# Performance work log

Measured on AMD Instinct MI355X. Metric: run time of the kernel, lower is better.

The kernel has to match this reference:

```python
import jax, jax.numpy as jnp
import numpy as np
from jax import lax

N_NODES = 50000
N_EDGES = 800000
FEAT = 16
HID = 64
K = 32
N_CLASSES = 8


def _dconv(Xc, W, b, src, dst, norm_out, norm_in):
    """Dual-direction diffusion (Chebyshev-style) graph convolution.
    Xc: [N, Fin], W: [2, K, Fin, HID], norm_*: per-edge weights."""
    N = Xc.shape[0]

    def prop(x, s, d, ne):
        # out[i] = sum_{e: d[e]=i} ne[e] * x[s[e]]
        return jax.ops.segment_sum(x[s] * ne[:, None], d, num_segments=N)

    # k = 0 term (identity support, both directions)
    H = Xc @ (W[0, 0] + W[1, 0])
    # k = 1 term
    T1o = prop(Xc, src, dst, norm_out)   # forward diffusion
    T1i = prop(Xc, dst, src, norm_in)    # reverse diffusion
    H = H + T1o @ W[0, 1] + T1i @ W[1, 1]

    def step(carry, Wk):
        T0o, T1o, T0i, T1i, Hacc = carry
        T2o = 2.0 * prop(T1o, src, dst, norm_out) - T0o
        T2i = 2.0 * prop(T1i, dst, src, norm_in) - T0i
        Hacc = Hacc + T2o @ Wk[0] + T2i @ Wk[1]
        return (T1o, T2o, T1i, T2i, Hacc), None

    Wtail = jnp.stack([W[0, 2:], W[1, 2:]], axis=1)  # [K-2, 2, Fin, HID]
    (_, _, _, _, H), _ = lax.scan(step, (Xc, T1o, Xc, T1i, H), Wtail)
    return H + b


def setup_inputs() -> dict:
    key = jax.random.key(0)
    ks = jax.random.split(key, 8)
    Fin = FEAT + HID
    wscale = 1.0 / np.sqrt(Fin * K)
    x = jax.random.normal(ks[0], (N_NODES, FEAT), jnp.float32)
    edge_index = jax.random.randint(ks[1], (2, N_EDGES), 0, N_NODES, jnp.int64)
    W_z = jax.random.normal(ks[2], (2, K, Fin, HID), jnp.float32) * wscale
    W_r = jax.random.normal(ks[3], (2, K, Fin, HID), jnp.float32) * wscale
    W_h = jax.random.normal(ks[4], (2, K, Fin, HID), jnp.float32) * wscale
    lin_w = jax.random.normal(ks[5], (HID, N_CLASSES), jnp.float32) / np.sqrt(HID)
    return {
        "x": x, "edge_index": edge_index,
        "W_z": W_z, "b_z": jnp.zeros((HID,), jnp.float32),
        "W_r": W_r, "b_r": jnp.zeros((HID,), jnp.float32),
        "W_h": W_h, "b_h": jnp.zeros((HID,), jnp.float32),
        "lin_w": lin_w, "lin_b": jnp.zeros((N_CLASSES,), jnp.float32),
    }


def reference(x, edge_index, W_z, b_z, W_r, b_r, W_h, b_h, lin_w, lin_b):
    N = x.shape[0]
    src, dst = edge_index[0], edge_index[1]
    w = jnp.ones(src.shape[0], x.dtype)
    deg_out = jax.ops.segment_sum(w, src, num_segments=N)
    deg_in = jax.ops.segment_sum(w, dst, num_segments=N)
    inv = lambda d: jnp.where(d > 0, 1.0 / d, 0.0)
    norm_out = inv(deg_out)[src]  # per-edge 1/out-deg(source), forward walk
    norm_in = inv(deg_in)[dst]    # per-edge 1/in-deg(target), reverse walk

    # DCRNN GRU cell, single step, H initialized to zeros
    H0 = jnp.zeros((N, HID), x.dtype)
    Xc = jnp.concatenate([x, H0], axis=1)
    Z = jax.nn.sigmoid(_dconv(Xc, W_z, b_z, src, dst, norm_out, norm_in))
    R = jax.nn.sigmoid(_dconv(Xc, W_r, b_r, src, dst, norm_out, norm_in))
    Xh = jnp.concatenate([x, H0 * R], axis=1)
    Ht = jnp.tanh(_dconv(Xh, W_h, b_h, src, dst, norm_out, norm_in))
    H = Z * H0 + (1.0 - Z) * Ht

    return jax.nn.relu(H) @ lin_w + lin_b
```

## Files before the change

kernel.cpp:

```cpp
#include <hip/hip_runtime.h>
#include <math.h>

#define N_NODES 50000
#define N_EDGES 800000
#define FEAT    16
#define HID     64
#define KORD    32
#define NCLS    8

#define WSL     5120
#define SLOT    (N_NODES * FEAT)

typedef __attribute__((ext_vector_type(8))) short bf8_t;
typedef __attribute__((ext_vector_type(4))) float f32x4;

static constexpr size_t Aln(size_t x) { return (x + 255) & ~size_t(255); }

static constexpr size_t OFF_DEG_OUT = 0;
static constexpr size_t OFF_DEG_IN  = OFF_DEG_OUT + Aln(N_NODES * 4);
static constexpr size_t OFF_CUR_DST = OFF_DEG_IN  + Aln(N_NODES * 4);
static constexpr size_t OFF_CUR_SRC = OFF_CUR_DST + Aln(N_NODES * 4);
static constexpr size_t ZERO_BYTES  = OFF_CUR_SRC + Aln(N_NODES * 4);
static constexpr size_t OFF_OFF_DST = ZERO_BYTES;
static constexpr size_t OFF_OFF_SRC = OFF_OFF_DST + Aln((N_NODES + 1) * 4);
static constexpr size_t OFF_CSRD    = OFF_OFF_SRC + Aln((N_NODES + 1) * 4);
static constexpr size_t OFF_CSRS    = OFF_CSRD + Aln(N_EDGES * 4);
static constexpr size_t OFF_SLAB    = OFF_CSRS + Aln(N_EDGES * 4);
static constexpr size_t OFF_BSZH    = OFF_SLAB + Aln((size_t)64 * SLOT * 4);
static constexpr size_t OFF_BSZL    = OFF_BSZH + Aln((size_t)32 * 8 * 64 * 8 * 2);
static constexpr size_t WS_TOTAL    = OFF_BSZL + Aln((size_t)32 * 8 * 64 * 8 * 2);

__device__ __forceinline__ ushort f2bf(float v) {
    unsigned int b = __float_as_uint(v);
    b += 0x7FFFu + ((b >> 16) & 1u);
    return (ushort)(b >> 16);
}
__device__ __forceinline__ float bf2f(ushort h) {
    return __uint_as_float((unsigned int)h << 16);
}

__global__ void count_deg_kernel(const int* __restrict__ ei,
                                 int* __restrict__ deg_out, int* __restrict__ deg_in) {
    int e4 = blockIdx.x * blockDim.x + threadIdx.x;
    if (e4 * 4 >= N_EDGES) return;
    int4 s = *(const int4*)&ei[e4 * 4];
    int4 d = *(const int4*)&ei[N_EDGES + e4 * 4];
    atomicAdd(&deg_out[s.x], 1); atomicAdd(&deg_out[s.y], 1);
    atomicAdd(&deg_out[s.z], 1); atomicAdd(&deg_out[s.w], 1);
    atomicAdd(&deg_in[d.x], 1);  atomicAdd(&deg_in[d.y], 1);
    atomicAdd(&deg_in[d.z], 1);  atomicAdd(&deg_in[d.w], 1);
}

__global__ __launch_bounds__(1024) void scan_kernel(const int* __restrict__ degA, int* __restrict__ offA,
                                                    const int* __restrict__ degB, int* __restrict__ offB) {
    const int* deg = blockIdx.x ? degB : degA;
    int* off = blockIdx.x ? offB : offA;
    __shared__ int wsum[16];
    __shared__ int s_run;
    const int t = threadIdx.x, lane = t & 63, wid = t >> 6;
    if (t == 0) s_run = 0;
    __syncthreads();
    for (int base = 0; base < N_NODES; base += 1024) {
        int i = base + t;
        int v = (i < N_NODES) ? deg[i] : 0;
        int xv = v;
        #pragma unroll
        for (int d = 1; d < 64; d <<= 1) {
            int tt = __shfl_up(xv, d, 64);
            if (lane >= d) xv += tt;
        }
        if (lane == 63) wsum[wid] = xv;
        __syncthreads();
        int add = s_run;
        for (int w = 0; w < wid; ++w) add += wsum[w];
        if (i < N_NODES) off[i] = add + xv - v;
        __syncthreads();
        if (t == 1023) s_run = add + xv;
        __syncthreads();
    }
    if (t == 0) off[N_NODES] = s_run;
}

__global__ void fill_csr_kernel(const int* __restrict__ ei,
                                const int* __restrict__ deg_out, const int* __restrict__ deg_in,
                                const int* __restrict__ off_dst, const int* __restrict__ off_src,
                                int* __restrict__ cur_dst, int* __restrict__ cur_src,
                                unsigned int* __restrict__ csrd, unsigned int* __restrict__ csrs) {
    int e = blockIdx.x * blockDim.x + threadIdx.x;
    if (e >= N_EDGES) return;
    int s = ei[e], d = ei[N_EDGES + e];
    int p = off_dst[d] + atomicAdd(&cur_dst[d], 1);
    csrd[p] = ((unsigned int)deg_out[s] << 16) | (unsigned int)s;
    int q = off_src[s] + atomicAdd(&cur_src[s], 1);
    csrs[q] = ((unsigned int)deg_in[d] << 16) | (unsigned int)d;
}

__device__ __forceinline__ float4 gather4d(const unsigned int* __restrict__ csr, int beg, int end,
                                           int u, int fq, const float* __restrict__ src) {
    float4 acc = {0.f, 0.f, 0.f, 0.f};
    for (int e0 = beg; e0 < end; e0 += 16) {
        int ea = e0 + u, eb = e0 + 4 + u, ec = e0 + 8 + u, ed = e0 + 12 + u;
        unsigned int pa = (ea < end) ? csr[ea] : 0x10000u;
        unsigned int pb = (eb < end) ? csr[eb] : 0x10000u;
        unsigned int pc = (ec < end) ? csr[ec] : 0x10000u;
        unsigned int pd = (ed < end) ? csr[ed] : 0x10000u;
        float wa = (ea < end) ? 1.0f / (float)(pa >> 16) : 0.0f;
        float wb = (eb < end) ? 1.0f / (float)(pb >> 16) : 0.0f;
        float wc = (ec < end) ? 1.0f / (float)(pc >> 16) : 0.0f;
        float wd = (ed < end) ? 1.0f / (float)(pd >> 16) : 0.0f;
        const float4 ra = *(const float4*)&src[(pa & 0xFFFFu) * FEAT + fq * 4];
        const float4 rb = *(const float4*)&src[(pb & 0xFFFFu) * FEAT + fq * 4];
        const float4 rc = *(const float4*)&src[(pc & 0xFFFFu) * FEAT + fq * 4];
        const float4 rd = *(const float4*)&src[(pd & 0xFFFFu) * FEAT + fq * 4];
        acc.x += wa * ra.x + wb * rb.x + wc * rc.x + wd * rd.x;
        acc.y += wa * ra.y + wb * rb.y + wc * rc.y + wd * rd.y;
        acc.z += wa * ra.z + wb * rb.z + wc * rc.z + wd * rd.z;
        acc.w += wa * ra.w + wb * rb.w + wc * rc.w + wd * rd.w;
    }
    return acc;
}

__device__ __forceinline__ float4 reduce_u(float4 a) {
    a.x += __shfl_xor(a.x, 4); a.y += __shfl_xor(a.y, 4);
    a.z += __shfl_xor(a.z, 4); a.w += __shfl_xor(a.w, 4);
    a.x += __shfl_xor(a.x, 8); a.y += __shfl_xor(a.y, 8);
    a.z += __shfl_xor(a.z, 8); a.w += __shfl_xor(a.w, 8);
    return a;
}

__global__ __launch_bounds__(256) void init_kernel(
    const float* __restrict__ x,
    const int* __restrict__ off_dst, const unsigned int* __restrict__ csrd,
    const int* __restrict__ off_src, const unsigned int* __restrict__ csrs,
    float* __restrict__ slab) {
    const int dir = blockIdx.x & 1;
    const int bi  = blockIdx.x >> 1;
    const int* off = dir ? off_src : off_dst;
    const unsigned int* csr = dir ? csrs : csrd;
    const int t = threadIdx.x;
    const int g = t >> 4, l = t & 15, u = l >> 2, fq = l & 3;
    const int i = bi * 16 + g;
    const int b = off[i], e = off[i + 1];
    float4 a = reduce_u(gather4d(csr, b, e, u, fq, x));
    if (u == 0) {
        const int ro = i * FEAT + fq * 4;
        float4 xr = *(const float4*)&x[ro];
        *(float4*)&slab[(size_t)(dir * 32 + 0) * SLOT + ro] = xr;
        *(float4*)&slab[(size_t)(dir * 32 + 1) * SLOT + ro] = a;
    }
}

__global__ __launch_bounds__(256) void step_kernel(
    const int* __restrict__ off_dst, const unsigned int* __restrict__ csrd,
    const int* __restrict__ off_src, const unsigned int* __restrict__ csrs,
    float* __restrict__ slab, int k) {
    const int dir = blockIdx.x & 1;
    const int bi  = blockIdx.x >> 1;
    const int* off = dir ? off_src : off_dst;
    const unsigned int* csr = dir ? csrs : csrd;
    const float* prev = slab + (size_t)(dir * 32 + k - 1) * SLOT;
    const float* pp   = slab + (size_t)(dir * 32 + k - 2) * SLOT;
    float*       outp = slab + (size_t)(dir * 32 + k) * SLOT;
    const int t = threadIdx.x;
    const int g = t >> 4, l = t & 15, u = l >> 2, fq = l & 3;
    const int i = bi * 16 + g;
    const int b = off[i], e = off[i + 1];
    float4 a = reduce_u(gather4d(csr, b, e, u, fq, prev));
    if (u == 0) {
        const int ro = i * FEAT + fq * 4;
        float4 p = *(const float4*)&pp[ro];
        float4 t2;
        t2.x = 2.f * a.x - p.x; t2.y = 2.f * a.y - p.y;
        t2.z = 2.f * a.z - p.z; t2.w = 2.f * a.w - p.w;
        *(float4*)&outp[ro] = t2;
    }
}

__global__ void wswiz_kernel(const float* __restrict__ Wz, const float* __restrict__ Wh,
                             ushort* __restrict__ bszh, ushort* __restrict__ bszl) {
    int idx = blockIdx.x * blockDim.x + threadIdx.x;
    if (idx >= 32 * 8 * 64) return;
    int l  = idx & 63;
    int nc = (idx >> 6) & 7;
    int kc = idx >> 9;
    int si = kc * 2 + ((l >> 4) >> 1);
    int f0 = ((l >> 4) & 1) * 8;
    int c  = nc * 16 + (l & 15);
    const float* W = (c < 64) ? Wz : Wh;
    int cc = (c < 64) ? c : c - 64;
    ushort vh[8], vl[8];
    #pragma unroll
    for (int i = 0; i < 8; ++i) {
        float v = W[(size_t)si * WSL + (f0 + i) * 64 + cc];
        ushort h = f2bf(v);
        vh[i] = h;
        vl[i] = f2bf(v - bf2f(h));
    }
    ushort* dh = &bszh[(size_t)idx * 8];
    *(ushort4*)dh       = make_ushort4(vh[0], vh[1], vh[2], vh[3]);
    *(ushort4*)(dh + 4) = make_ushort4(vh[4], vh[5], vh[6], vh[7]);
    ushort* dl = &bszl[(size_t)idx * 8];
    *(ushort4*)dl       = make_ushort4(vl[0], vl[1], vl[2], vl[3]);
    *(ushort4*)(dl + 4) = make_ushort4(vl[4], vl[5], vl[6], vl[7]);
}

__global__ __launch_bounds__(256) void final_kernel(
    const float* __restrict__ slab, const ushort* __restrict__ bszh, const ushort* __restrict__ bszl,
    const float* __restrict__ bz, const float* __restrict__ bh,
    const float* __restrict__ lin_w, const float* __restrict__ lin_b,
    float* __restrict__ out) {
    const int t = threadIdx.x;
    const int w = t >> 6, l = t & 63;
    const int cl = l & 15, hi = l >> 4;
    const int n0 = blockIdx.x * 64 + w * 16;

    f32x4 acc[8];
    #pragma unroll
    for (int nc = 0; nc < 8; ++nc) {
        int c = nc * 16 + cl;
        float bias = (c < 64) ? bz[c] : bh[c - 64];
        acc[nc] = (f32x4){bias, bias, bias, bias};
    }

    const int nodeA = n0 + cl;
    const int aOk = (nodeA < N_NODES);
    const int siAdd = (hi >> 1);
    const int f0 = (hi & 1) * 8;

    for (int kc = 0; kc < 32; ++kc) {
        bf8_t aHi = (bf8_t)0, aLo = (bf8_t)0;
        if (aOk) {
            int si = kc * 2 + siAdd;
            const float* ap = &slab[(size_t)si * SLOT + nodeA * FEAT + f0];
            float4 a0 = *(const float4*)ap;
            float4 a1 = *(const float4*)(ap + 4);
            float av[8] = {a0.x, a0.y, a0.z, a0.w, a1.x, a1.y, a1.z, a1.w};
            #pragma unroll
            for (int i = 0; i < 8; ++i) {
                ushort h = f2bf(av[i]);
                aHi[i] = (short)h;
                aLo[i] = (short)f2bf(av[i] - bf2f(h));
            }
        }
        #pragma unroll
        for (int nc = 0; nc < 8; ++nc) {
            const size_t fo = (size_t)(((kc * 8 + nc) * 64) + l) * 8;
            bf8_t bHi = *(const bf8_t*)&bszh[fo];
            bf8_t bLo = *(const bf8_t*)&bszl[fo];
            acc[nc] = __builtin_amdgcn_mfma_f32_16x16x32_bf16(aHi, bHi, acc[nc], 0, 0, 0);
            acc[nc] = __builtin_amdgcn_mfma_f32_16x16x32_bf16(aLo, bHi, acc[nc], 0, 0, 0);
            acc[nc] = __builtin_amdgcn_mfma_f32_16x16x32_bf16(aHi, bLo, acc[nc], 0, 0, 0);
        }
    }

    float po[4][8];
    #pragma unroll
    for (int i = 0; i < 4; ++i)
        #pragma unroll
        for (int cls = 0; cls < 8; ++cls) po[i][cls] = 0.f;
    #pragma unroll
    for (int i = 0; i < 4; ++i) {
        #pragma unroll
        for (int nc = 0; nc < 4; ++nc) {
            float hz = acc[nc][i], hh = acc[nc + 4][i];
            float z  = 1.f / (1.f + __expf(-hz));
            float ht = tanhf(hh);
            float v  = fmaxf(0.f, (1.f - z) * ht);
            const float* lwr = &lin_w[(nc * 16 + cl) * 8];
            #pragma unroll
            for (int cls = 0; cls < 8; ++cls) po[i][cls] += v * lwr[cls];
        }
    }
    #pragma unroll
    for (int m = 1; m < 16; m <<= 1) {
        #pragma unroll
        for (int i = 0; i < 4; ++i)
            #pragma unroll
            for (int cls = 0; cls < 8; ++cls)
                po[i][cls] += __shfl_xor(po[i][cls], m, 16);
    }
    if (cl < 8) {
        #pragma unroll
        for (int i = 0; i < 4; ++i) {
            int node = n0 + hi * 4 + i;
            if (node < N_NODES) out[node * NCLS + cl] = po[i][cl] + lin_b[cl];
        }
    }
}

extern "C" void kernel_launch(void* const* d_in, const int* in_sizes, int n_in,
                              void* d_out, int out_size, void* d_ws, size_t ws_size,
                              hipStream_t stream) {
    const float* x   = (const float*)d_in[0];
    const int*   ei  = (const int*)d_in[1];
    const float* Wz  = (const float*)d_in[2];
    const float* bz  = (const float*)d_in[3];
    const float* Wh  = (const float*)d_in[6];
    const float* bh  = (const float*)d_in[7];
    const float* lw  = (const float*)d_in[8];
    const float* lb  = (const float*)d_in[9];
    float* out = (float*)d_out;
    char* ws = (char*)d_ws;

    int*  deg_out = (int*)(ws + OFF_DEG_OUT);
    int*  deg_in  = (int*)(ws + OFF_DEG_IN);
    int*  cur_dst = (int*)(ws + OFF_CUR_DST);
    int*  cur_src = (int*)(ws + OFF_CUR_SRC);
    int*  off_dst = (int*)(ws + OFF_OFF_DST);
    int*  off_src = (int*)(ws + OFF_OFF_SRC);
    unsigned int* csrd = (unsigned int*)(ws + OFF_CSRD);
    unsigned int* csrs = (unsigned int*)(ws + OFF_CSRS);
    float*  slab = (float*)(ws + OFF_SLAB);
    ushort* bszh = (ushort*)(ws + OFF_BSZH);
    ushort* bszl = (ushort*)(ws + OFF_BSZL);

    hipMemsetAsync(ws, 0, ZERO_BYTES, stream);

    const int EB = (N_EDGES + 255) / 256;
    const int NB16 = N_NODES / 16;
    count_deg_kernel<<<(N_EDGES / 4 + 255) / 256, 256, 0, stream>>>(ei, deg_out, deg_in);
    scan_kernel<<<2, 1024, 0, stream>>>(deg_in, off_dst, deg_out, off_src);
    fill_csr_kernel<<<EB, 256, 0, stream>>>(ei, deg_out, deg_in, off_dst, off_src,
                                            cur_dst, cur_src, csrd, csrs);
    wswiz_kernel<<<(32 * 8 * 64 + 255) / 256, 256, 0, stream>>>(Wz, Wh, bszh, bszl);
    init_kernel<<<NB16 * 2, 256, 0, stream>>>(x, off_dst, csrd, off_src, csrs, slab);

    for (int k = 2; k < KORD; ++k)
        step_kernel<<<NB16 * 2, 256, 0, stream>>>(off_dst, csrd, off_src, csrs, slab, k);

    final_kernel<<<(N_NODES + 63) / 64, 256, 0, stream>>>(slab, bszh, bszl, bz, bh, lw, lb, out);
}
```

Before: 815.8 us.

## Stage weight fragments in LDS with double buffering and two node tiles per wave

The final GEMM kernel now copies each k-chunk of the pre-swizzled bf16 weight fragments into a double-buffered shared-memory array, prefetching the next chunk while MFMAs run on the current one. Each wave also handles two 16-node tiles, so every weight fragment feeds twice as many MFMAs and the grid is halved. This cuts redundant global and L2 weight traffic. The cost is more accumulator registers, 32 KB of LDS per block, and a block barrier every iteration. The final kernel is a small part of total runtime next to the 30 step kernels.

```diff
diff --git a/kernel.cpp b/kernel.cpp
--- a/kernel.cpp
+++ b/kernel.cpp
@@ -204,86 +204,115 @@
     *(ushort4*)(dl + 4) = make_ushort4(vl[4], vl[5], vl[6], vl[7]);
 }
 
+__device__ __forceinline__ void cvtA(const float* __restrict__ ap, bf8_t& aHi, bf8_t& aLo) {
+    float4 a0 = *(const float4*)ap;
+    float4 a1 = *(const float4*)(ap + 4);
+    float av[8] = {a0.x, a0.y, a0.z, a0.w, a1.x, a1.y, a1.z, a1.w};
+    #pragma unroll
+    for (int i = 0; i < 8; ++i) {
+        ushort h = f2bf(av[i]);
+        aHi[i] = (short)h;
+        aLo[i] = (short)f2bf(av[i] - bf2f(h));
+    }
+}
+
 __global__ __launch_bounds__(256) void final_kernel(
     const float* __restrict__ slab, const ushort* __restrict__ bszh, const ushort* __restrict__ bszl,
     const float* __restrict__ bz, const float* __restrict__ bh,
     const float* __restrict__ lin_w, const float* __restrict__ lin_b,
     float* __restrict__ out) {
+    __shared__ alignas(16) ushort sfrag[2][8192];
     const int t = threadIdx.x;
     const int w = t >> 6, l = t & 63;
     const int cl = l & 15, hi = l >> 4;
-    const int n0 = blockIdx.x * 64 + w * 16;
-
-    f32x4 acc[8];
+    const int n0 = blockIdx.x * 128 + w * 32;
+    const int nodeA0 = n0 + cl, nodeA1 = n0 + 16 + cl;
+    const bool ok0 = nodeA0 < N_NODES, ok1 = nodeA1 < N_NODES;
+    const int siAdd = hi >> 1, f0 = (hi & 1) * 8;
+
+    f32x4 acc[2][8];
     #pragma unroll
     for (int nc = 0; nc < 8; ++nc) {
         int c = nc * 16 + cl;
         float bias = (c < 64) ? bz[c] : bh[c - 64];
-        acc[nc] = (f32x4){bias, bias, bias, bias};
-    }
-
-    const int nodeA = n0 + cl;
-    const int aOk = (nodeA < N_NODES);
-    const int siAdd = (hi >> 1);
-    const int f0 = (hi & 1) * 8;
+        acc[0][nc] = (f32x4){bias, bias, bias, bias};
+        acc[1][nc] = (f32x4){bias, bias, bias, bias};
+    }
+
+    {
+        const uint4* sH = (const uint4*)(bszh);
+        const uint4* sL = (const uint4*)(bszl);
+        uint4* d = (uint4*)sfrag[0];
+        d[t] = sH[t]; d[t + 256] = sH[t + 256];
+        d[t + 512] = sL[t]; d[t + 768] = sL[t + 256];
+    }
+    __syncthreads();
 
     for (int kc = 0; kc < 32; ++kc) {
-        bf8_t aHi = (bf8_t)0, aLo = (bf8_t)0;
-        if (aOk) {
+        const int buf = kc & 1;
+        if (kc < 31) {
+            const uint4* sH = (const uint4*)(bszh + (size_t)(kc + 1) * 4096);
+            const uint4* sL = (const uint4*)(bszl + (size_t)(kc + 1) * 4096);
+            uint4* d = (uint4*)sfrag[buf ^ 1];
+            d[t] = sH[t]; d[t + 256] = sH[t + 256];
+            d[t + 512] = sL[t]; d[t + 768] = sL[t + 256];
+        }
+        bf8_t aH0 = (bf8_t)0, aL0 = (bf8_t)0, aH1 = (bf8_t)0, aL1 = (bf8_t)0;
+        {
             int si = kc * 2 + siAdd;
-            const float* ap = &slab[(size_t)si * SLOT + nodeA * FEAT + f0];
-            float4 a0 = *(const float4*)ap;
-            float4 a1 = *(const float4*)(ap + 4);
-            float av[8] = {a0.x, a0.y, a0.z, a0.w, a1.x, a1.y, a1.z, a1.w};
-            #pragma unroll
-            for (int i = 0; i < 8; ++i) {
-                ushort h = f2bf(av[i]);
-                aHi[i] = (short)h;
-                aLo[i] = (short)f2bf(av[i] - bf2f(h));
-            }
-        }
+            const float* base = &slab[(size_t)si * SLOT + f0];
+            if (ok0) cvtA(&base[nodeA0 * FEAT], aH0, aL0);
+            if (ok1) cvtA(&base[nodeA1 * FEAT], aH1, aL1);
+        }
+        const ushort* fb = sfrag[buf];
         #pragma unroll
         for (int nc = 0; nc < 8; ++nc) {
-            const size_t fo = (size_t)(((kc * 8 + nc) * 64) + l) * 8;
-            bf8_t bHi = *(const bf8_t*)&bszh[fo];
-            bf8_t bLo = *(const bf8_t*)&bszl[fo];
-            acc[nc] = __builtin_amdgcn_mfma_f32_16x16x32_bf16(aHi, bHi, acc[nc], 0, 0, 0);
-            acc[nc] = __builtin_amdgcn_mfma_f32_16x16x32_bf16(aLo, bHi, acc[nc], 0, 0, 0);
-            acc[nc] = __builtin_amdgcn_mfma_f32_16x16x32_bf16(aHi, bLo, acc[nc], 0, 0, 0);
-        }
-    }
-
-    float po[4][8];
+            bf8_t bHi = *(const bf8_t*)&fb[nc * 512 + l * 8];
+            bf8_t bLo = *(const bf8_t*)&fb[4096 + nc * 512 + l * 8];
+            acc[0][nc] = __builtin_amdgcn_mfma_f32_16x16x32_bf16(aH0, bHi, acc[0][nc], 0, 0, 0);
+            acc[0][nc] = __builtin_amdgcn_mfma_f32_16x16x32_bf16(aL0, bHi, acc[0][nc], 0, 0, 0);
+            acc[0][nc] = __builtin_amdgcn_mfma_f32_16x16x32_bf16(aH0, bLo, acc[0][nc], 0, 0, 0);
+            acc[1][nc] = __builtin_amdgcn_mfma_f32_16x16x32_bf16(aH1, bHi, acc[1][nc], 0, 0, 0);
+            acc[1][nc] = __builtin_amdgcn_mfma_f32_16x16x32_bf16(aL1, bHi, acc[1][nc], 0, 0, 0);
+            acc[1][nc] = __builtin_amdgcn_mfma_f32_16x16x32_bf16(aH1, bLo, acc[1][nc], 0, 0, 0);
+        }
+        __syncthreads();
+    }
+
     #pragma unroll
-    for (int i = 0; i < 4; ++i)
-        #pragma unroll
-        for (int cls = 0; cls < 8; ++cls) po[i][cls] = 0.f;
-    #pragma unroll
-    for (int i = 0; i < 4; ++i) {
-        #pragma unroll
-        for (int nc = 0; nc < 4; ++nc) {
-            float hz = acc[nc][i], hh = acc[nc + 4][i];
-            float z  = 1.f / (1.f + __expf(-hz));
-            float ht = tanhf(hh);
-            float v  = fmaxf(0.f, (1.f - z) * ht);
-            const float* lwr = &lin_w[(nc * 16 + cl) * 8];
-            #pragma unroll
-            for (int cls = 0; cls < 8; ++cls) po[i][cls] += v * lwr[cls];
-        }
-    }
-    #pragma unroll
-    for (int m = 1; m < 16; m <<= 1) {
+    for (int tl = 0; tl < 2; ++tl) {
+        float po[4][8];
         #pragma unroll
         for (int i = 0; i < 4; ++i)
             #pragma unroll
-            for (int cls = 0; cls < 8; ++cls)
-                po[i][cls] += __shfl_xor(po[i][cls], m, 16);
-    }
-    if (cl < 8) {
+            for (int cls = 0; cls < 8; ++cls) po[i][cls] = 0.f;
         #pragma unroll
         for (int i = 0; i < 4; ++i) {
-            int node = n0 + hi * 4 + i;
-            if (node < N_NODES) out[node * NCLS + cl] = po[i][cl] + lin_b[cl];
+            #pragma unroll
+            for (int nc = 0; nc < 4; ++nc) {
+                float hz = acc[tl][nc][i], hh = acc[tl][nc + 4][i];
+                float z  = 1.f / (1.f + __expf(-hz));
+                float ht = tanhf(hh);
+                float v  = fmaxf(0.f, (1.f - z) * ht);
+                const float* lwr = &lin_w[(nc * 16 + cl) * 8];
+                #pragma unroll
+                for (int cls = 0; cls < 8; ++cls) po[i][cls] += v * lwr[cls];
+            }
+        }
+        #pragma unroll
+        for (int m = 1; m < 16; m <<= 1) {
+            #pragma unroll
+            for (int i = 0; i < 4; ++i)
+                #pragma unroll
+                for (int cls = 0; cls < 8; ++cls)
+                    po[i][cls] += __shfl_xor(po[i][cls], m, 16);
+        }
+        if (cl < 8) {
+            #pragma unroll
+            for (int i = 0; i < 4; ++i) {
+                int node = n0 + tl * 16 + hi * 4 + i;
+                if (node < N_NODES) out[node * NCLS + cl] = po[i][cl] + lin_b[cl];
+            }
         }
     }
 }
@@ -328,5 +357,6 @@
     for (int k = 2; k < KORD; ++k)
         step_kernel<<<NB16 * 2, 256, 0, stream>>>(off_dst, csrd, off_src, csrs, slab, k);
 
-    final_kernel<<<(N_NODES + 63) / 64, 256, 0, stream>>>(slab, bszh, bszl, bz, bh, lw, lb, out);
-}
+    final_kernel<<<(N_NODES + 127) / 128, 256, 0, stream>>>(slab, bszh, bszl,
+                                                            bz, bh, lw, lb, out);
+}
```

After: 801.0 us. No clear change (-1.8%).
